# Kernel optimization log

Hardware: AMD Instinct MI355X
Metric: run time of the kernel (lower is better)

## Reference

```python
import jax, jax.numpy as jnp
import numpy as np
from jax import lax

K = 3          # kernel_size
G = 8          # group count in SIFA
EPS = 1e-5     # BN and GN eps


def _bn(x, g, b, m, v):
    # eval-mode BatchNorm2d over channel dim 1
    scale = (g / jnp.sqrt(v + EPS))[None, :, None, None]
    shift = (b - m * g / jnp.sqrt(v + EPS))[None, :, None, None]
    return x * scale + shift


def setup_inputs() -> dict:
    key = jax.random.key(0)
    ks = jax.random.split(key, 20)
    B, C, H, W, OUP = 8, 64, 128, 128, 128
    CE = C * K * K  # expanded channels = 576
    CG = C // G     # channels per group view = 8
    f32 = jnp.float32
    inp = {
        "x": jax.random.normal(ks[0], (B, C, H, W), f32),
        # depthwise generate conv: groups=C, out=C*K^2 -> OIHW [CE,1,K,K]
        "gen_w": jax.random.normal(ks[1], (CE, 1, K, K), f32) * 0.1,
        "gen_bn_g": jnp.ones((CE,), f32) + 0.1 * jax.random.normal(ks[2], (CE,), f32),
        "gen_bn_b": 0.1 * jax.random.normal(ks[3], (CE,), f32),
        "gen_bn_m": 0.05 * jax.random.normal(ks[4], (CE,), f32),
        "gen_bn_v": jax.random.uniform(ks[5], (CE,), f32, 0.5, 1.5),
        # GroupNorm(num_groups=CG, num_channels=CG) affine params
        "gn_w": jnp.ones((CG,), f32) + 0.1 * jax.random.normal(ks[6], (CG,), f32),
        "gn_b": 0.1 * jax.random.normal(ks[7], (CG,), f32),
        # gating params, shape (1, CG, 1, 1)
        "cweight": 0.1 * jax.random.normal(ks[8], (1, CG, 1, 1), f32),
        "cbias": jnp.ones((1, CG, 1, 1), f32) + 0.1 * jax.random.normal(ks[9], (1, CG, 1, 1), f32),
        "sweight": 0.1 * jax.random.normal(ks[10], (1, CG, 1, 1), f32),
        "sbias": jnp.ones((1, CG, 1, 1), f32) + 0.1 * jax.random.normal(ks[11], (1, CG, 1, 1), f32),
        "weights_add": jnp.asarray(0.5, f32),
        # final Conv: C -> OUP, k=K, s=K, p=0, bias=False + BN + SiLU
        "conv_w": jax.random.normal(ks[12], (OUP, C, K, K), f32) * (1.0 / np.sqrt(C * K * K)),
        "conv_bn_g": jnp.ones((OUP,), f32) + 0.1 * jax.random.normal(ks[13], (OUP,), f32),
        "conv_bn_b": 0.1 * jax.random.normal(ks[14], (OUP,), f32),
        "conv_bn_m": 0.05 * jax.random.normal(ks[15], (OUP,), f32),
        "conv_bn_v": jax.random.uniform(ks[16], (OUP,), f32, 0.5, 1.5),
    }
    return inp


def reference(x, gen_w, gen_bn_g, gen_bn_b, gen_bn_m, gen_bn_v,
              gn_w, gn_b, cweight, cbias, sweight, sbias, weights_add,
              conv_w, conv_bn_g, conv_bn_b, conv_bn_m, conv_bn_v):
    B, C, H, W = x.shape
    # --- generate: depthwise conv (groups=C) + BN + ReLU ---
    y = lax.conv_general_dilated(
        x, gen_w, window_strides=(1, 1), padding=[(K // 2, K // 2)] * 2,
        feature_group_count=C,
        dimension_numbers=("NCHW", "OIHW", "NCHW"))  # [B, C*K*K, H, W]
    y = jax.nn.relu(_bn(y, gen_bn_g, gen_bn_b, gen_bn_m, gen_bn_v))
    # --- rearrange 'b c (n1 n2) h w -> b c (h n1) (w n2)' ---
    y = y.reshape(B, C, K, K, H, W)          # (b, c, n1, n2, h, w)
    y = y.transpose(0, 1, 4, 2, 5, 3)        # (b, c, h, n1, w, n2)
    HK, WK = H * K, W * K
    y = y.reshape(B, C, HK, WK)
    # --- group view: (b*G, C//G, HK, WK) ---
    g = y.reshape(B * G, C // G, HK, WK)
    # channel gate: global avg pool -> affine -> sigmoid
    x_ch = jnp.mean(g, axis=(2, 3), keepdims=True)        # [B*G, CG, 1, 1]
    ch = g * jax.nn.sigmoid(cweight * x_ch + cbias)
    # spatial gate: per-channel GroupNorm (num_groups == num_channels)
    mu = jnp.mean(g, axis=(2, 3), keepdims=True)
    var = jnp.var(g, axis=(2, 3), keepdims=True)
    gnorm = (g - mu) / jnp.sqrt(var + EPS)
    gnorm = gnorm * gn_w[None, :, None, None] + gn_b[None, :, None, None]
    sp = g * jax.nn.sigmoid(sweight * gnorm + sbias)
    out = weights_add * ch + (1.0 - weights_add) * sp
    out = out.reshape(B, C, HK, WK)
    # --- final Conv: k=K, s=K, p=0, no bias + BN + SiLU ---
    z = lax.conv_general_dilated(
        out, conv_w, window_strides=(K, K), padding="VALID",
        dimension_numbers=("NCHW", "OIHW", "NCHW"))       # [B, OUP, H, W]
    z = _bn(z, conv_bn_g, conv_bn_b, conv_bn_m, conv_bn_v)
    return z * jax.nn.sigmoid(z)  # SiLU
```

## Files before the change

### kernel.cpp

```cpp
#include <hip/hip_runtime.h>
#include <math.h>


#define EPSF 1e-5f
typedef _Float16 v8h __attribute__((ext_vector_type(8)));
typedef __fp16 fp16x2 __attribute__((ext_vector_type(2)));
typedef float v4f __attribute__((ext_vector_type(4)));

static constexpr int C_ = 64, HW_ = 16384, W_ = 128;
static constexpr int KB_ = 80;

static constexpr int WS_WFOLD = 0;
static constexpr int WS_SHIFT = 5184;
static constexpr int WS_BIAS  = 5760;
static constexpr int WS_GATE  = 5888;
static constexpr int WS_PART  = 7936;
static constexpr int WS_WH    = 73472;
static constexpr int WS_BIMG  = 114688;
static constexpr size_t BIMG_BATCH_F16 = (size_t)128 * KB_ * 128 * 8;
static constexpr size_t BIMG_BATCH_FLT = BIMG_BATCH_F16 / 2;

__device__ __forceinline__ float sigmf(float v) { return 1.f / (1.f + __expf(-v)); }

__device__ __forceinline__ unsigned int pk_u32(float a, float b) {
    fp16x2 h = __builtin_amdgcn_cvt_pkrtz(a, b);
    return __builtin_bit_cast(unsigned int, h);
}

__global__ __launch_bounds__(256) void k_fold(
    const float* __restrict__ gen_w,
    const float* __restrict__ gg, const float* __restrict__ gb,
    const float* __restrict__ gm, const float* __restrict__ gv,
    const float* __restrict__ conv_w,
    const float* __restrict__ cg, const float* __restrict__ cb,
    const float* __restrict__ cm, const float* __restrict__ cv,
    float* __restrict__ ws)
{
    int idx = blockIdx.x * 256 + threadIdx.x;
    _Float16* Whp = (_Float16*)(ws + WS_WH);
    if (idx < 81920) {
        int kb = idx >> 10, oup = (idx >> 3) & 127, e = idx & 7;
        int k = kb * 8 + e;
        int grp = k / 80, rr = k - grp * 80;
        int tp = rr / 40, vv = rr - tp * 40;
        float v = 0.f;
        if (vv < 36) {
            int j = vv >> 2, cl = vv & 3, c = grp * 8 + tp * 4 + cl;
            float s = cg[oup] * rsqrtf(cv[oup] + EPSF);
            v = conv_w[(oup * C_ + c) * 9 + j] * s;
        }
        Whp[idx] = (_Float16)v;
    } else if (idx < 87104) {
        int i = idx - 81920; int ce = i / 9;
        float s = gg[ce] * rsqrtf(gv[ce] + EPSF);
        ws[WS_WFOLD + i] = gen_w[i] * s;
    } else if (idx < 87680) {
        int ce = idx - 87104;
        float s = gg[ce] * rsqrtf(gv[ce] + EPSF);
        ws[WS_SHIFT + ce] = gb[ce] - gm[ce] * s;
    } else if (idx < 87808) {
        int oup = idx - 87680;
        float s = cg[oup] * rsqrtf(cv[oup] + EPSF);
        ws[WS_BIAS + oup] = cb[oup] - cm[oup] * s;
    }
}

__global__ __launch_bounds__(256) void k_conv(
    const float* __restrict__ x, float* __restrict__ ws, int b0)
{
    __shared__ float xs[4][18 * 19];
    __shared__ unsigned int ul[256 * 22];
    __shared__ float red[4][8];
    int bid = blockIdx.x;
    int cq = bid & 15, p = (bid >> 4) & 63, bbl = bid >> 10;
    int b = b0 + bbl;
    int oh0 = (p >> 3) << 4, ow0 = (p & 7) << 4;
    int t = threadIdx.x;
    int row16 = t >> 4, col = t & 15;

    for (int i = t; i < 1296; i += 256) {
        int ch = i / 324, rr = i - ch * 324;
        int r = rr / 18, cc = rr - r * 18;
        int yy = oh0 + r - 1, xx = ow0 + cc - 1;
        float v = 0.f;
        if (yy >= 0 && yy < 128 && xx >= 0 && xx < 128)
            v = x[(size_t)(b * C_ + cq * 4 + ch) * HW_ + yy * 128 + xx];
        xs[ch][r * 19 + cc] = v;
    }
    __syncthreads();

    float nb4[4][9];
#pragma unroll
    for (int ch = 0; ch < 4; ++ch)
#pragma unroll
        for (int dy = 0; dy < 3; ++dy)
#pragma unroll
            for (int dx = 0; dx < 3; ++dx)
                nb4[ch][dy * 3 + dx] = xs[ch][(row16 + dy) * 19 + col + dx];

    float st[8];
#pragma unroll
    for (int k = 0; k < 8; ++k) st[k] = 0.f;

#pragma unroll 1
    for (int j = 0; j < 9; ++j) {
        float wj[4][9], sj[4];
#pragma unroll
        for (int ch = 0; ch < 4; ++ch) {
            const float* wp = ws + WS_WFOLD + (cq * 4 + ch) * 81 + j * 9;
#pragma unroll
            for (int k = 0; k < 9; ++k) wj[ch][k] = wp[k];
            sj[ch] = ws[WS_SHIFT + (cq * 4 + ch) * 9 + j];
        }
        float uv[4];
#pragma unroll
        for (int ch = 0; ch < 4; ++ch) {
            float a = sj[ch];
#pragma unroll
            for (int k = 0; k < 9; ++k) a = fmaf(wj[ch][k], nb4[ch][k], a);
            float v = fmaxf(a, 0.f);
            uv[ch] = v;
            st[ch * 2] += v;
            st[ch * 2 + 1] = fmaf(v, v, st[ch * 2 + 1]);
        }
        uint2 pk;
        pk.x = pk_u32(uv[0], uv[1]);
        pk.y = pk_u32(uv[2], uv[3]);
        int ci = j >> 1;
        *(uint2*)&ul[t * 22 + ci * 4 + (j & 1) * 2] = pk;
    }
    {
        uint2 z; z.x = 0u; z.y = 0u;
        *(uint2*)&ul[t * 22 + 18] = z;
    }

    int tile = ((p >> 3) * 2 + (row16 >> 3)) * 8 + (p & 7);
    int px = (row16 & 7) * 16 + col;
    int kbBase = (cq >> 1) * 10 + (cq & 1) * 5;
    _Float16* Bimg = (_Float16*)(ws + WS_BIMG) + (size_t)bbl * BIMG_BATCH_F16;
#pragma unroll
    for (int ci = 0; ci < 5; ++ci) {
        uint2 lo = *(uint2*)&ul[t * 22 + ci * 4];
        uint2 hi = *(uint2*)&ul[t * 22 + ci * 4 + 2];
        uint4 cell; cell.x = lo.x; cell.y = lo.y; cell.z = hi.x; cell.w = hi.y;
        *(uint4*)(Bimg + (size_t)(tile * KB_ + kbBase + ci) * 1024 + (size_t)px * 8) = cell;
    }

#pragma unroll
    for (int off = 32; off > 0; off >>= 1)
#pragma unroll
        for (int k = 0; k < 8; ++k) st[k] += __shfl_down(st[k], off, 64);
    int w = t >> 6, lane = t & 63;
    if (lane == 0)
#pragma unroll
        for (int k = 0; k < 8; ++k) red[w][k] = st[k];
    __syncthreads();
    if (t < 8) {
        float v = red[0][t] + red[1][t] + red[2][t] + red[3][t];
        float* part = ws + WS_PART;
        part[(size_t)((b * 16 + cq) * 8 + t) * 64 + p] = v;
    }
}

__global__ __launch_bounds__(256) void k_gate(
    const float* __restrict__ part,
    const float* __restrict__ cwt, const float* __restrict__ cbs,
    const float* __restrict__ swt, const float* __restrict__ sbs,
    const float* __restrict__ gnw, const float* __restrict__ gnb,
    const float* __restrict__ wadd, float4* __restrict__ gate, int b0, int nb)
{
    int i = blockIdx.x * 256 + threadIdx.x;
    if (i >= nb * 64) return;
    int b = b0 + (i >> 6), c = i & 63;
    const float* pp = part + (size_t)((b * 16 + (c >> 2)) * 8 + (c & 3) * 2) * 64;
    float s1 = 0.f, s2 = 0.f;
#pragma unroll
    for (int q = 0; q < 16; ++q) {
        float4 a = *(const float4*)(pp + q * 4);
        float4 d = *(const float4*)(pp + 64 + q * 4);
        s1 += a.x + a.y + a.z + a.w;
        s2 += d.x + d.y + d.z + d.w;
    }
    const float N = 9.f * 16384.f;
    float mean = s1 / N;
    float var = s2 / N - mean * mean;
    float inv = rsqrtf(var + EPSF);
    int cgi = c & 7;
    float wa = wadd[0];
    float cgt = sigmf(cwt[cgi] * mean + cbs[cgi]);
    const float NL2E = -1.44269504f;
    float4 o;
    o.x = wa * cgt;
    o.y = 1.f - wa;
    o.z = NL2E * (swt[cgi] * gnw[cgi] * inv);
    o.w = NL2E * (swt[cgi] * (gnb[cgi] - mean * inv * gnw[cgi]) + sbs[cgi]);
    gate[b * 64 + c] = o;
}

__global__ __launch_bounds__(256) void k_gapply(float* __restrict__ ws, int b0)
{
    int kb = blockIdx.x >> 1, h = blockIdx.x & 1, bbl = blockIdx.y;
    int b = b0 + bbl;
    int grp = kb / 10, r = kb - grp * 10, tp = r / 5;
    int cbase = grp * 8 + tp * 4;
    const float4* gp = (const float4*)(ws + WS_GATE);
    float4 g0 = gp[b * 64 + cbase];
    float4 g1 = gp[b * 64 + cbase + 1];
    float4 g2 = gp[b * 64 + cbase + 2];
    float4 g3 = gp[b * 64 + cbase + 3];
    _Float16* base = (_Float16*)(ws + WS_BIMG) + (size_t)bbl * BIMG_BATCH_F16
                   + (size_t)kb * 1024;
    int t = threadIdx.x;
    int tsub = t >> 7;
    int off = (t & 127) * 8;
#pragma unroll 1
    for (int i = 0; i < 32; ++i) {
        int tl = h * 64 + i * 2 + tsub;
        _Float16* p = base + (size_t)tl * (KB_ * 1024) + off;
        v8h v = *(const v8h*)p;
        float u[8];
#pragma unroll
        for (int e = 0; e < 8; ++e) {
            float f = (float)v[e];
            float4 g = (e & 3) == 0 ? g0 : ((e & 3) == 1 ? g1 : ((e & 3) == 2 ? g2 : g3));
            float ex = __builtin_amdgcn_exp2f(fmaf(g.z, f, g.w));
            u[e] = f * fmaf(g.y, __builtin_amdgcn_rcpf(1.f + ex), g.x);
        }
        uint2 lo, hi;
        lo.x = pk_u32(u[0], u[1]);
        lo.y = pk_u32(u[2], u[3]);
        hi.x = pk_u32(u[4], u[5]);
        hi.y = pk_u32(u[6], u[7]);
        uint4 cell; cell.x = lo.x; cell.y = lo.y; cell.z = hi.x; cell.w = hi.y;
        *(uint4*)p = cell;
    }
}

__global__ __launch_bounds__(256, 4) void k_main(
    const float* __restrict__ ws, float* __restrict__ out, int b0)
{
    __shared__ float bias_s[128];
    int t = threadIdx.x;
    int bid = blockIdx.x;
    int bbl = bid >> 7, tile = bid & 127;
    int b = b0 + bbl;
    int oh0 = (tile >> 3) << 3, ow0 = (tile & 7) << 4;
    if (t < 128) bias_s[t] = ws[WS_BIAS + t];
    __syncthreads();

    int w = __builtin_amdgcn_readfirstlane(t >> 6);
    int lane = t & 63, quad = lane >> 4, l15 = lane & 15;
    int arow = ((w & 1) << 6) + l15;
    int brow = ((w >> 1) << 6) + l15;

    const _Float16* Aq = (const _Float16*)(ws + WS_WH)
        + (size_t)quad * 1024 + (size_t)arow * 8;
    const _Float16* Bq = (const _Float16*)(ws + WS_BIMG)
        + (size_t)bbl * BIMG_BATCH_F16 + (size_t)tile * (KB_ * 1024)
        + (size_t)quad * 1024 + (size_t)brow * 8;

    v4f acc[4][4];
#pragma unroll
    for (int a = 0; a < 4; ++a)
#pragma unroll
        for (int bb = 0; bb < 4; ++bb) acc[a][bb] = (v4f)0.f;

    v8h A[4], B0[4], B1[4];
    auto LDA = [&](int s) {
        size_t o = (size_t)s << 12;
#pragma unroll
        for (int a = 0; a < 4; ++a) A[a] = *(const v8h*)(Aq + o + a * 128);
    };
    auto LDB = [&](int s, v8h* B) {
        size_t o = (size_t)s << 12;
#pragma unroll
        for (int bb = 0; bb < 4; ++bb) B[bb] = *(const v8h*)(Bq + o + bb * 128);
    };
    auto MM = [&](v8h* B) {
#pragma unroll
        for (int a = 0; a < 4; ++a)
#pragma unroll
            for (int bb = 0; bb < 4; ++bb)
                acc[a][bb] = __builtin_amdgcn_mfma_f32_16x16x32_f16(A[a], B[bb], acc[a][bb], 0, 0, 0);
    };

    LDB(0, B0);
#pragma unroll 1
    for (int s = 0; s < 18; s += 2) {
        LDB(s + 1, B1);
        LDA(s);
        MM(B0);
        LDB(s + 2, B0);
        LDA(s + 1);
        MM(B1);
    }
    LDB(19, B1);
    LDA(18); MM(B0);
    LDA(19); MM(B1);

    size_t ob = (size_t)b * 128 * HW_;
#pragma unroll
    for (int a = 0; a < 4; ++a) {
#pragma unroll
        for (int r = 0; r < 4; ++r) {
            int oup = ((w & 1) << 6) + (a << 4) + (quad << 2) + r;
            float bo = bias_s[oup];
#pragma unroll
            for (int bb = 0; bb < 4; ++bb) {
                int p2 = ((w >> 1) << 6) + (bb << 4) + l15;
                int py2 = p2 >> 4, px2 = p2 & 15;
                float z = acc[a][bb][r] + bo;
                out[ob + (size_t)oup * HW_ + (oh0 + py2) * W_ + ow0 + px2] = z * sigmf(z);
            }
        }
    }
}

extern "C" void kernel_launch(void* const* d_in, const int* in_sizes, int n_in,
                              void* d_out, int out_size, void* d_ws, size_t ws_size,
                              hipStream_t stream)
{
    const float* x      = (const float*)d_in[0];
    const float* gen_w  = (const float*)d_in[1];
    const float* gg     = (const float*)d_in[2];
    const float* gb     = (const float*)d_in[3];
    const float* gm     = (const float*)d_in[4];
    const float* gv     = (const float*)d_in[5];
    const float* gnw    = (const float*)d_in[6];
    const float* gnb    = (const float*)d_in[7];
    const float* cwt    = (const float*)d_in[8];
    const float* cbs    = (const float*)d_in[9];
    const float* swt    = (const float*)d_in[10];
    const float* sbs    = (const float*)d_in[11];
    const float* wadd   = (const float*)d_in[12];
    const float* conv_w = (const float*)d_in[13];
    const float* cg2    = (const float*)d_in[14];
    const float* cb2    = (const float*)d_in[15];
    const float* cm2    = (const float*)d_in[16];
    const float* cv2    = (const float*)d_in[17];
    float* ws  = (float*)d_ws;
    float* out = (float*)d_out;

    size_t avail = ws_size / 4;
    int nb = 1;
    const int cands[4] = {8, 4, 2, 1};
    for (int i = 0; i < 4; ++i) {
        if ((size_t)WS_BIMG + (size_t)cands[i] * BIMG_BATCH_FLT <= avail) { nb = cands[i]; break; }
    }

    k_fold<<<343, 256, 0, stream>>>(gen_w, gg, gb, gm, gv, conv_w, cg2, cb2, cm2, cv2, ws);
    for (int b0 = 0; b0 < 8; b0 += nb) {
        k_conv<<<nb * 1024, 256, 0, stream>>>(x, ws, b0);
        k_gate<<<(nb * 64 + 255) / 256, 256, 0, stream>>>(
            ws + WS_PART, cwt, cbs, swt, sbs, gnw, gnb, wadd,
            (float4*)(ws + WS_GATE), b0, nb);
        k_gapply<<<dim3(160, nb), 256, 0, stream>>>(ws, b0);
        k_main<<<nb * 128, 256, 0, stream>>>(ws, out, b0);
    }
}
```

Before: 282.7 us.

## Fuse gate application into GEMM kernel via LDS staging of B tiles

Removes the separate k_gapply pass, which read and rewrote the whole fp16 expanded image in global memory. k_main now loads raw B tiles, applies the channel/spatial gate in registers and stages the gated tile in shared memory before the MFMA loop. Each tile is split into two halves of 64 pixels, giving twice as many blocks, each computing all 128 output channels. In exchange it adds LDS traffic and barriers, loses the global-load/MFMA software pipelining, and reloads the A weights once per half-tile block.

```diff
diff --git a/kernel.cpp b/kernel.cpp
--- a/kernel.cpp
+++ b/kernel.cpp
@@ -197,119 +197,89 @@
     gate[b * 64 + c] = o;
 }
 
-__global__ __launch_bounds__(256) void k_gapply(float* __restrict__ ws, int b0)
-{
-    int kb = blockIdx.x >> 1, h = blockIdx.x & 1, bbl = blockIdx.y;
-    int b = b0 + bbl;
-    int grp = kb / 10, r = kb - grp * 10, tp = r / 5;
-    int cbase = grp * 8 + tp * 4;
-    const float4* gp = (const float4*)(ws + WS_GATE);
-    float4 g0 = gp[b * 64 + cbase];
-    float4 g1 = gp[b * 64 + cbase + 1];
-    float4 g2 = gp[b * 64 + cbase + 2];
-    float4 g3 = gp[b * 64 + cbase + 3];
-    _Float16* base = (_Float16*)(ws + WS_BIMG) + (size_t)bbl * BIMG_BATCH_F16
-                   + (size_t)kb * 1024;
-    int t = threadIdx.x;
-    int tsub = t >> 7;
-    int off = (t & 127) * 8;
-#pragma unroll 1
-    for (int i = 0; i < 32; ++i) {
-        int tl = h * 64 + i * 2 + tsub;
-        _Float16* p = base + (size_t)tl * (KB_ * 1024) + off;
-        v8h v = *(const v8h*)p;
-        float u[8];
-#pragma unroll
-        for (int e = 0; e < 8; ++e) {
-            float f = (float)v[e];
-            float4 g = (e & 3) == 0 ? g0 : ((e & 3) == 1 ? g1 : ((e & 3) == 2 ? g2 : g3));
-            float ex = __builtin_amdgcn_exp2f(fmaf(g.z, f, g.w));
-            u[e] = f * fmaf(g.y, __builtin_amdgcn_rcpf(1.f + ex), g.x);
-        }
-        uint2 lo, hi;
-        lo.x = pk_u32(u[0], u[1]);
-        lo.y = pk_u32(u[2], u[3]);
-        hi.x = pk_u32(u[4], u[5]);
-        hi.y = pk_u32(u[6], u[7]);
-        uint4 cell; cell.x = lo.x; cell.y = lo.y; cell.z = hi.x; cell.w = hi.y;
-        *(uint4*)p = cell;
-    }
-}
-
 __global__ __launch_bounds__(256, 4) void k_main(
     const float* __restrict__ ws, float* __restrict__ out, int b0)
 {
-    __shared__ float bias_s[128];
+    __shared__ _Float16 Bs[40 * 512];
     int t = threadIdx.x;
     int bid = blockIdx.x;
-    int bbl = bid >> 7, tile = bid & 127;
+    int half = bid & 1, tile = (bid >> 1) & 127, bbl = bid >> 8;
     int b = b0 + bbl;
     int oh0 = (tile >> 3) << 3, ow0 = (tile & 7) << 4;
-    if (t < 128) bias_s[t] = ws[WS_BIAS + t];
-    __syncthreads();
 
     int w = __builtin_amdgcn_readfirstlane(t >> 6);
     int lane = t & 63, quad = lane >> 4, l15 = lane & 15;
-    int arow = ((w & 1) << 6) + l15;
-    int brow = ((w >> 1) << 6) + l15;
-
-    const _Float16* Aq = (const _Float16*)(ws + WS_WH)
-        + (size_t)quad * 1024 + (size_t)arow * 8;
-    const _Float16* Bq = (const _Float16*)(ws + WS_BIMG)
+
+    const _Float16* Wh = (const _Float16*)(ws + WS_WH);
+    const _Float16* Bimg = (const _Float16*)(ws + WS_BIMG)
         + (size_t)bbl * BIMG_BATCH_F16 + (size_t)tile * (KB_ * 1024)
-        + (size_t)quad * 1024 + (size_t)brow * 8;
-
-    v4f acc[4][4];
-#pragma unroll
-    for (int a = 0; a < 4; ++a)
+        + (size_t)(half * 64 + lane) * 8;
+    const float4* gp = (const float4*)(ws + WS_GATE) + b * 64;
+
+    v4f acc[2][4];
+#pragma unroll
+    for (int a = 0; a < 2; ++a)
 #pragma unroll
         for (int bb = 0; bb < 4; ++bb) acc[a][bb] = (v4f)0.f;
 
-    v8h A[4], B0[4], B1[4];
-    auto LDA = [&](int s) {
-        size_t o = (size_t)s << 12;
-#pragma unroll
-        for (int a = 0; a < 4; ++a) A[a] = *(const v8h*)(Aq + o + a * 128);
-    };
-    auto LDB = [&](int s, v8h* B) {
-        size_t o = (size_t)s << 12;
-#pragma unroll
-        for (int bb = 0; bb < 4; ++bb) B[bb] = *(const v8h*)(Bq + o + bb * 128);
-    };
-    auto MM = [&](v8h* B) {
-#pragma unroll
-        for (int a = 0; a < 4; ++a)
+#pragma unroll 1
+    for (int r = 0; r < 2; ++r) {
+        if (r) __syncthreads();
+#pragma unroll 2
+        for (int i = 0; i < 10; ++i) {
+            int kl = i * 4 + w;
+            int kb = r * 40 + kl;
+            int q5 = kb / 10;
+            int cbase = q5 * 8 + (kb - q5 * 10 >= 5 ? 4 : 0);
+            float4 g0 = gp[cbase], g1 = gp[cbase + 1];
+            float4 g2 = gp[cbase + 2], g3 = gp[cbase + 3];
+            uint4 cell = *(const uint4*)(Bimg + (size_t)kb * 1024);
+            v8h v = __builtin_bit_cast(v8h, cell);
+            float u[8];
+#pragma unroll
+            for (int e = 0; e < 8; ++e) {
+                float f = (float)v[e];
+                float4 g = (e & 3) == 0 ? g0 : ((e & 3) == 1 ? g1 : ((e & 3) == 2 ? g2 : g3));
+                float ex = __builtin_amdgcn_exp2f(fmaf(g.z, f, g.w));
+                u[e] = f * fmaf(g.y, __builtin_amdgcn_rcpf(1.f + ex), g.x);
+            }
+            uint4 oc;
+            oc.x = pk_u32(u[0], u[1]); oc.y = pk_u32(u[2], u[3]);
+            oc.z = pk_u32(u[4], u[5]); oc.w = pk_u32(u[6], u[7]);
+            *(uint4*)(Bs + kl * 512 + lane * 8) = oc;
+        }
+        __syncthreads();
+#pragma unroll
+        for (int s = 0; s < 10; ++s) {
+            int cglob = r * 40 + s * 4 + quad;
+            const _Float16* Ap = Wh + ((size_t)cglob * 128 + w * 32 + l15) * 8;
+            v8h A0 = *(const v8h*)(Ap);
+            v8h A1 = *(const v8h*)(Ap + 128);
+            int klq = s * 4 + quad;
+            v8h Bf[4];
 #pragma unroll
             for (int bb = 0; bb < 4; ++bb)
-                acc[a][bb] = __builtin_amdgcn_mfma_f32_16x16x32_f16(A[a], B[bb], acc[a][bb], 0, 0, 0);
-    };
-
-    LDB(0, B0);
-#pragma unroll 1
-    for (int s = 0; s < 18; s += 2) {
-        LDB(s + 1, B1);
-        LDA(s);
-        MM(B0);
-        LDB(s + 2, B0);
-        LDA(s + 1);
-        MM(B1);
-    }
-    LDB(19, B1);
-    LDA(18); MM(B0);
-    LDA(19); MM(B1);
+                Bf[bb] = *(const v8h*)(Bs + klq * 512 + (bb * 16 + l15) * 8);
+#pragma unroll
+            for (int bb = 0; bb < 4; ++bb) {
+                acc[0][bb] = __builtin_amdgcn_mfma_f32_16x16x32_f16(A0, Bf[bb], acc[0][bb], 0, 0, 0);
+                acc[1][bb] = __builtin_amdgcn_mfma_f32_16x16x32_f16(A1, Bf[bb], acc[1][bb], 0, 0, 0);
+            }
+        }
+    }
 
     size_t ob = (size_t)b * 128 * HW_;
 #pragma unroll
-    for (int a = 0; a < 4; ++a) {
-#pragma unroll
-        for (int r = 0; r < 4; ++r) {
-            int oup = ((w & 1) << 6) + (a << 4) + (quad << 2) + r;
-            float bo = bias_s[oup];
+    for (int a = 0; a < 2; ++a) {
+#pragma unroll
+        for (int r2 = 0; r2 < 4; ++r2) {
+            int oup = w * 32 + a * 16 + quad * 4 + r2;
+            float bo = ws[WS_BIAS + oup];
 #pragma unroll
             for (int bb = 0; bb < 4; ++bb) {
-                int p2 = ((w >> 1) << 6) + (bb << 4) + l15;
+                int p2 = half * 64 + bb * 16 + l15;
                 int py2 = p2 >> 4, px2 = p2 & 15;
-                float z = acc[a][bb][r] + bo;
+                float z = acc[a][bb][r2] + bo;
                 out[ob + (size_t)oup * HW_ + (oh0 + py2) * W_ + ow0 + px2] = z * sigmf(z);
             }
         }
@@ -354,7 +324,6 @@
         k_gate<<<(nb * 64 + 255) / 256, 256, 0, stream>>>(
             ws + WS_PART, cwt, cbs, swt, sbs, gnw, gnb, wadd,
             (float4*)(ws + WS_GATE), b0, nb);
-        k_gapply<<<dim3(160, nb), 256, 0, stream>>>(ws, b0);
-        k_main<<<nb * 128, 256, 0, stream>>>(ws, out, b0);
-    }
-}
+        k_main<<<nb * 256, 256, 0, stream>>>(ws, out, b0);
+    }
+}
```

Result: faster. 236.7 us (-16.3%).
